# Kernel tuning notes

Hardware: AMD Instinct MI355X
Metric: run time of the kernel (lower is better)

## Reference

```python
import numpy as np
import jax
import jax.numpy as jnp
from collections import deque

NUM_CLASSES = 32
N_PARENTS = 4
N_CHILD = 7
SINK_WEIGHT = 0.1
EPS = 1e-7
B, D, H, W = 2, 96, 96, 96

# ---- static tree construction (mirrors adjacency_matrix / bitpack_tree / reachability) ----

def _build_adjacency():
    n = NUM_CLASSES + 1  # node 0 is the virtual root
    A = np.zeros((n, n), dtype=np.int64)
    for p in range(N_PARENTS):
        A[0, 1 + p] = 1
        for c in range(N_CHILD):
            A[1 + p, 1 + N_PARENTS + p * N_CHILD + c] = 1
    return A

ADJ = _build_adjacency()

def _reachability(A):
    # R[i, j] = 1 iff j is reachable from i (i is ancestor-or-self of j)
    R = np.eye(A.shape[0], dtype=bool) | (A > 0)
    for _ in range(A.shape[0]):
        Rn = R | (R @ (A > 0))
        if (Rn == R).all():
            break
        R = Rn
    return R

def _bitpack(A):
    # each node's bitmask encodes its path from the root; (x & group) == class tests descendant-ness
    n = A.shape[0]
    bc = np.zeros(n, dtype=np.int64)
    bg = np.zeros(n, dtype=np.int64)
    bit = 0
    q = deque([0])
    while q:
        p = q.popleft()
        ch = np.nonzero(A[p])[0]
        if len(ch) == 0:
            continue
        w = int(np.ceil(np.log2(len(ch) + 1)))
        for i, c in enumerate(ch):
            bc[c] = bc[p] | ((i + 1) << bit)
            bg[c] = bg[p] | (((1 << w) - 1) << bit)
            q.append(c)
        bit += w
    return bc, bg

_BC, _BG = _bitpack(ADJ)
BM_CLASS = _BC[1:].astype(np.int32)
BM_GROUP = _BG[1:].astype(np.int32)
RMT = _reachability(ADJ)[1:, 1:].T.astype(np.float32)  # RMT[label, c] = c is ancestor-or-self
LEAF = np.nonzero(ADJ[1:, 1:].sum(axis=1) == 0)[0].astype(np.int32)
_SIB = ((ADJ.T @ ADJ) > 0)[1:, 1:]
SINK_IDS = [N_PARENTS + p * N_CHILD for p in range(N_PARENTS)]
PARENT_OF = {s: int(ADJ[1:, 1:][:, s].argmax()) for s in SINK_IDS}
SIBS = {}
for _s in SINK_IDS:
    _row = _SIB[_s].copy()
    _row[_s] = False
    SIBS[_s] = np.nonzero(_row)[0].tolist()
# DDESC[l, c] = 1 iff class l is a descendant-or-self of class c (bitmask test)
DDESC = ((BM_CLASS[:, None] & BM_GROUP[None, :]) == BM_CLASS[None, :]).astype(np.float32)


def setup_inputs() -> dict:
    key = jax.random.key(0)
    k1, k2 = jax.random.split(key)
    images = jax.random.normal(k1, (B, NUM_CLASSES, D, H, W), dtype=jnp.float32)
    targets = jax.random.randint(k2, (B, D, H, W), 0, NUM_CLASSES, dtype=jnp.int32)
    masks = jnp.ones((B, NUM_CLASSES), dtype=bool)
    return {"images": images, "targets": targets, "masks": masks}


def reference(images, targets, masks):
    C = NUM_CLASSES
    probs = jax.nn.softmax(images, axis=1)  # activation_fn over class dim
    leaf = jnp.asarray(LEAF)
    pred = leaf[jnp.argmax(probs[:, LEAF], axis=1)]  # _argmax_leaves -> [B,D,H,W] int32
    bm_class = jnp.asarray(BM_CLASS)
    rmt = jnp.asarray(RMT)
    ddesc = jnp.asarray(DDESC)

    def per_sample(p, pr, y, m):
        p = p.reshape(C, -1).T          # [N, C] probabilities
        y = y.reshape(-1)
        pr = pr.reshape(-1)
        valid = y != 255
        vw = valid.astype(p.dtype)
        y_safe = jnp.where(valid, y, 0).astype(jnp.int32)
        mf = m.astype(p.dtype)

        # ---- sink dice (hierarchical sink/sibling logic) ----
        pred_bm = bm_class[pr]
        sds, fls = [], []
        for s in SINK_IDS:
            sib_mask = jnp.zeros_like(valid)
            for sib in SIBS[s]:
                sib_mask = sib_mask | (y_safe == sib) | ((~m[sib]) & (pr == sib))
            par = PARENT_OF[s]
            pmask = (pred_bm & int(BM_GROUP[par])) == int(BM_CLASS[par])
            tgt = (pmask & (~sib_mask)).astype(p.dtype) * vw
            pp = p[:, s] * vw
            inter = jnp.sum(pp * tgt)
            d = 1.0 - (2.0 * inter + 1e-5) / (jnp.sum(pp) + jnp.sum(tgt) + 1e-5)
            sds.append(d)
            fls.append((jnp.sum(sib_mask & valid) > 0).astype(p.dtype))
        sd = jnp.stack(sds)
        fl = jnp.stack(fls)
        cnt = fl.sum()
        sink_dice = SINK_WEIGHT * jnp.where(cnt > 0, jnp.sum(sd * fl) / jnp.maximum(cnt, 1.0), 0.0)

        # ---- main dice (smooth_nr=0) + hierarchical CE over masked classes ----
        t = rmt[y_safe]                 # [N, C] multi-hot (label + ancestors)
        wcol = vw[:, None]
        inter = jnp.sum(p * t * wcol, axis=0)
        denom = jnp.sum(p * wcol, axis=0) + jnp.sum(t * wcol, axis=0)
        dice_c = 1.0 - (2.0 * inter) / (denom + 1e-5)
        dice = jnp.sum(dice_c * mf) / jnp.maximum(mf.sum(), 1.0)

        logp = jnp.log(jnp.clip(p, EPS, 1.0 - EPS))
        ce = jnp.sum(-jnp.sum(t * logp * mf[None, :], axis=1) * vw) / jnp.maximum(vw.sum(), 1.0)

        # ---- confusion matrix via joint (pred, true) histogram + descendant matrix ----
        flat = pr.astype(jnp.int32) * C + y_safe
        hist = jnp.zeros((C * C,), p.dtype).at[flat].add(vw).reshape(C, C)  # [pred, true]
        tp = jnp.einsum('lc,lt,tc->c', ddesc, hist, ddesc)
        fp = jnp.einsum('lc,lt->c', ddesc, hist) - tp
        fn = jnp.einsum('lt,tc->c', hist, ddesc) - tp
        cm = jnp.stack([tp, fp, fn], axis=-1) * mf[:, None]
        return jnp.stack([ce, dice, sink_dice]), cm

    loss, cm = jax.vmap(per_sample)(probs, pred, targets, masks)
    return loss, cm, pred
```

## Files before the change

kernel.cpp:

```cpp
#include <hip/hip_runtime.h>

#define NC 32
#define NVOX (96*96*96)
#define NB 512
#define TPB 256
#define ROWS 33

#define WS_CE     0
#define WS_SP     32
#define WS_SPT    64
#define WS_SINKI  96
#define WS_SIB    100
#define WS_TGT    104
#define WS_HIST   128
#define SLOT_STRIDE 1152
#define NSLOT     (2 * NB)
#define FINAL_OFF (NSLOT * SLOT_STRIDE)
#define NCHUNK    8
#define BLK_PER_CH (NB / NCHUNK)

__device__ __forceinline__ float wave_reduce(float v) {
    #pragma unroll
    for (int off = 32; off > 0; off >>= 1)
        v += __shfl_down(v, off, 64);
    return v;
}

__global__ __launch_bounds__(TPB, 4) void voxel_kernel(
    const float* __restrict__ images,
    const int*   __restrict__ targets,
    const int*   __restrict__ masks,
    float* __restrict__ ws,
    float* __restrict__ pred_out)
{
    const int slot = blockIdx.x;
    const int b    = slot & 1;
    const int blk  = slot >> 1;
    const int tid  = threadIdx.x;

    __shared__ float s_e[TPB * ROWS];
    __shared__ float s_hist[NC * NC];
    __shared__ float s_spt[NC];
    __shared__ float s_mf[NC];
    __shared__ float s_red[45];

    for (int i = tid; i < NC * NC; i += TPB) s_hist[i] = 0.f;
    if (tid < 45) s_red[tid] = 0.f;
    if (tid < NC) {
        s_spt[tid] = 0.f;
        s_mf[tid]  = (masks[b * NC + tid] != 0) ? 1.f : 0.f;
    }
    __syncthreads();

    const float* img  = images + (size_t)b * NC * NVOX;
    const int*   tgt  = targets + (size_t)b * NVOX;
    float*       pout = pred_out + (size_t)b * NVOX;
    float*       wsb  = ws + (size_t)slot * SLOT_STRIDE;
    float*       et   = &s_e[tid * ROWS];

    float sp[NC];
    #pragma unroll
    for (int c = 0; c < NC; ++c) sp[c] = 0.f;
    float ce = 0.f;
    float sinkI[4] = {0.f, 0.f, 0.f, 0.f};
    float sibc[4]  = {0.f, 0.f, 0.f, 0.f};
    float tgtc[4]  = {0.f, 0.f, 0.f, 0.f};

    for (int v = blk * TPB + tid; v < NVOX; v += NB * TPB) {
        const int  y     = tgt[v];
        const bool valid = (y != 255);
        const int  ysafe = valid ? y : 0;
        const float vwf  = valid ? 1.f : 0.f;

        float sum  = 0.f;
        float best = -3.4e38f;
        int   pred = 4;
        #pragma unroll
        for (int c = 0; c < NC; ++c) {
            const float x  = img[(size_t)c * NVOX + v];
            const float ev = __expf(x);
            et[c] = ev;
            sum  += ev;
            if (c >= 4) {
                if (x > best) { best = x; pred = c; }
            }
        }
        const float rinv = 1.f / sum;
        pout[v] = (float)pred;

        const int pp = (pred - 4) / 7;
        const int py = (ysafe >= 4) ? (ysafe - 4) / 7 : -1;
        const int pyi = (py >= 0) ? py : 0;

        const float pyv  = et[ysafe] * rinv;
        const float ppv  = et[pyi] * rinv;
        const float eskv = et[4 + 7 * pp] * rinv;

        float term = __logf(fminf(fmaxf(pyv, 1e-7f), 1.f - 1e-7f)) * s_mf[ysafe];
        if (py >= 0)
            term += __logf(fminf(fmaxf(ppv, 1e-7f), 1.f - 1e-7f)) * s_mf[pyi];
        ce -= term * vwf;

        atomicAdd(&s_spt[ysafe], pyv * vwf);
        if (py >= 0) atomicAdd(&s_spt[pyi], ppv * vwf);

        atomicAdd(&s_hist[pred * NC + ysafe], vwf);

        const bool pm = (s_mf[pred] == 0.f);
        #pragma unroll
        for (int k = 0; k < 4; ++k) {
            const int  sk   = 4 + 7 * k;
            const bool ysib = (py == k) && (ysafe != sk);
            const bool msib = pm && (pp == k) && (pred != sk);
            const bool sib  = ysib || msib;
            if (sib && valid) sibc[k] += 1.f;
            if ((pp == k) && !sib && valid) {
                tgtc[k]  += 1.f;
                sinkI[k] += eskv;
            }
        }

        const float rw = rinv * vwf;
        #pragma unroll
        for (int c = 0; c < NC; ++c)
            sp[c] = __builtin_fmaf(et[c], rw, sp[c]);
    }

    const int lane = tid & 63;
    {
        float r = wave_reduce(ce);
        if (lane == 0) atomicAdd(&s_red[0], r);
    }
    #pragma unroll
    for (int c = 0; c < NC; ++c) {
        float r = wave_reduce(sp[c]);
        if (lane == 0) atomicAdd(&s_red[1 + c], r);
    }
    #pragma unroll
    for (int k = 0; k < 4; ++k) {
        float r = wave_reduce(sinkI[k]);
        if (lane == 0) atomicAdd(&s_red[33 + k], r);
        r = wave_reduce(sibc[k]);
        if (lane == 0) atomicAdd(&s_red[37 + k], r);
        r = wave_reduce(tgtc[k]);
        if (lane == 0) atomicAdd(&s_red[41 + k], r);
    }
    __syncthreads();

    for (int i = tid; i < NC * NC; i += TPB) wsb[WS_HIST + i] = s_hist[i];
    if (tid == 0) wsb[WS_CE] = s_red[0];
    if (tid < NC) {
        wsb[WS_SP  + tid] = s_red[1 + tid];
        wsb[WS_SPT + tid] = s_spt[tid];
    }
    if (tid < 4) {
        wsb[WS_SINKI + tid] = s_red[33 + tid];
        wsb[WS_SIB   + tid] = s_red[37 + tid];
        wsb[WS_TGT   + tid] = s_red[41 + tid];
    }
}

__global__ __launch_bounds__(TPB) void reduce_kernel(
    const float* __restrict__ ws, float* __restrict__ wsf)
{
    const int v = blockIdx.x * TPB + threadIdx.x;
    if (v >= 2 * SLOT_STRIDE) return;
    const int b   = v / SLOT_STRIDE;
    const int val = v % SLOT_STRIDE;
    const int blk0 = blockIdx.y * BLK_PER_CH;
    const float* base = ws + (size_t)b * SLOT_STRIDE + val;
    float s = 0.f;
    #pragma unroll 8
    for (int i = 0; i < BLK_PER_CH; ++i)
        s += base[(size_t)(2 * (blk0 + i)) * SLOT_STRIDE];
    atomicAdd(&wsf[v], s);
}

__global__ __launch_bounds__(64) void finalize_kernel(
    const float* __restrict__ wsf,
    const int*   __restrict__ masks,
    float* __restrict__ out)
{
    const int b = blockIdx.x;
    const float* wsb  = wsf + (size_t)b * SLOT_STRIDE;
    const float* hist = wsb + WS_HIST;
    const int tid = threadIdx.x;

    __shared__ float s_col[NC], s_row[NC], s_dice[NC], s_mf[NC];

    if (tid < NC) {
        float cs = 0.f, rs = 0.f;
        for (int j = 0; j < NC; ++j) {
            cs += hist[j * NC + tid];
            rs += hist[tid * NC + j];
        }
        s_col[tid] = cs;
        s_row[tid] = rs;
        s_mf[tid]  = (masks[b * NC + tid] != 0) ? 1.f : 0.f;
    }
    __syncthreads();

    if (tid < NC) {
        const int c = tid;
        float ycnt, pcnt, tp;
        if (c < 4) {
            int idx[8];
            idx[0] = c;
            for (int j = 0; j < 7; ++j) idx[1 + j] = 4 + 7 * c + j;
            ycnt = s_col[c]; pcnt = s_row[c];
            for (int j = 0; j < 7; ++j) { ycnt += s_col[idx[1 + j]]; pcnt += s_row[idx[1 + j]]; }
            tp = 0.f;
            for (int a = 0; a < 8; ++a)
                for (int d = 0; d < 8; ++d)
                    tp += hist[idx[a] * NC + idx[d]];
        } else {
            ycnt = s_col[c]; pcnt = s_row[c];
            tp = hist[c * NC + c];
        }
        const float mf = s_mf[c];
        out[6 + (b * NC + c) * 3 + 0] = tp * mf;
        out[6 + (b * NC + c) * 3 + 1] = (pcnt - tp) * mf;
        out[6 + (b * NC + c) * 3 + 2] = (ycnt - tp) * mf;
        float dc = 1.f - 2.f * wsb[WS_SPT + c] / (wsb[WS_SP + c] + ycnt + 1e-5f);
        s_dice[c] = dc * mf;
    }
    __syncthreads();

    if (tid == 0) {
        float vw = 0.f, dsum = 0.f, msum = 0.f;
        for (int c = 0; c < NC; ++c) {
            vw   += s_col[c];
            dsum += s_dice[c];
            msum += s_mf[c];
        }
        const float ce   = wsb[WS_CE] / fmaxf(vw, 1.f);
        const float dice = dsum / fmaxf(msum, 1.f);
        float cnt = 0.f, sd = 0.f;
        for (int k = 0; k < 4; ++k) {
            float fl = (wsb[WS_SIB + k] > 0.f) ? 1.f : 0.f;
            float d  = 1.f - (2.f * wsb[WS_SINKI + k] + 1e-5f) /
                             (wsb[WS_SP + 4 + 7 * k] + wsb[WS_TGT + k] + 1e-5f);
            cnt += fl;
            sd  += d * fl;
        }
        const float sink = (cnt > 0.f) ? 0.1f * (sd / fmaxf(cnt, 1.f)) : 0.f;
        out[b * 3 + 0] = ce;
        out[b * 3 + 1] = dice;
        out[b * 3 + 2] = sink;
    }
}

extern "C" void kernel_launch(void* const* d_in, const int* in_sizes, int n_in,
                              void* d_out, int out_size, void* d_ws, size_t ws_size,
                              hipStream_t stream) {
    const float* images  = (const float*)d_in[0];
    const int*   targets = (const int*)d_in[1];
    const int*   masks   = (const int*)d_in[2];
    float* out = (float*)d_out;
    float* ws  = (float*)d_ws;
    float* wsf = ws + FINAL_OFF;

    hipMemsetAsync(wsf, 0, 2 * SLOT_STRIDE * sizeof(float), stream);

    voxel_kernel<<<dim3(NSLOT), dim3(TPB), 0, stream>>>(
        images, targets, masks, ws, out + 6 + 2 * NC * 3);
    reduce_kernel<<<dim3((2 * SLOT_STRIDE + TPB - 1) / TPB, NCHUNK), dim3(TPB), 0, stream>>>(ws, wsf);
    finalize_kernel<<<dim3(2), dim3(64), 0, stream>>>(wsf, masks, out);
}
```

Measured before the change: 340.8 us.

## Keep softmax exponentials in registers and fuse finalize into reduce kernel

Drops the per-thread shared-memory exp buffer (33 floats per thread, about 33KB per block) and keeps the exponentials in a register array. The needed entries (target prob, parent prob, predicted sink prob) are picked up with selects inside the channel loop. This lifts the LDS limit on occupancy but raises register pressure. It also folds the finalize step into the reduce kernel using a last-block atomic counter, and moves the workspace zeroing into the voxel kernel, which removes a memset and a kernel launch.

```diff
diff --git a/kernel.cpp b/kernel.cpp
--- a/kernel.cpp
+++ b/kernel.cpp
@@ -4,7 +4,6 @@
 #define NVOX (96*96*96)
 #define NB 512
 #define TPB 256
-#define ROWS 33
 
 #define WS_CE     0
 #define WS_SP     32
@@ -16,8 +15,11 @@
 #define SLOT_STRIDE 1152
 #define NSLOT     (2 * NB)
 #define FINAL_OFF (NSLOT * SLOT_STRIDE)
+#define CTR_IDX   124
 #define NCHUNK    8
 #define BLK_PER_CH (NB / NCHUNK)
+#define RED_BLK_X ((2 * SLOT_STRIDE + TPB - 1) / TPB)
+#define RED_NBLK  (RED_BLK_X * NCHUNK)
 
 __device__ __forceinline__ float wave_reduce(float v) {
     #pragma unroll
@@ -38,7 +40,6 @@
     const int blk  = slot >> 1;
     const int tid  = threadIdx.x;
 
-    __shared__ float s_e[TPB * ROWS];
     __shared__ float s_hist[NC * NC];
     __shared__ float s_spt[NC];
     __shared__ float s_mf[NC];
@@ -50,13 +51,17 @@
         s_spt[tid] = 0.f;
         s_mf[tid]  = (masks[b * NC + tid] != 0) ? 1.f : 0.f;
     }
+    if (slot == 0) {
+        float* wsf = ws + FINAL_OFF;
+        for (int i = tid; i < 2 * SLOT_STRIDE; i += TPB) wsf[i] = 0.f;
+        if (tid == 0) *(unsigned int*)(ws + CTR_IDX) = 0u;
+    }
     __syncthreads();
 
     const float* img  = images + (size_t)b * NC * NVOX;
     const int*   tgt  = targets + (size_t)b * NVOX;
     float*       pout = pred_out + (size_t)b * NVOX;
     float*       wsb  = ws + (size_t)slot * SLOT_STRIDE;
-    float*       et   = &s_e[tid * ROWS];
 
     float sp[NC];
     #pragma unroll
@@ -71,30 +76,38 @@
         const bool valid = (y != 255);
         const int  ysafe = valid ? y : 0;
         const float vwf  = valid ? 1.f : 0.f;
-
-        float sum  = 0.f;
-        float best = -3.4e38f;
+        const int  py    = (ysafe >= 4) ? (ysafe - 4) / 7 : -1;
+        const int  pyi   = (py >= 0) ? py : 0;
+
+        float ev[NC];
+        float sum = 0.f, best = -3.4e38f;
+        float pyv_e = 0.f, ppv_e = 0.f, cur = 0.f, esk = 0.f;
         int   pred = 4;
         #pragma unroll
         for (int c = 0; c < NC; ++c) {
-            const float x  = img[(size_t)c * NVOX + v];
-            const float ev = __expf(x);
-            et[c] = ev;
-            sum  += ev;
+            const float x = img[(size_t)c * NVOX + v];
+            const float e = __expf(x);
+            ev[c] = e;
+            sum  += e;
+            pyv_e = (c == ysafe) ? e : pyv_e;
+            if (c < 4)
+                ppv_e = (c == pyi) ? e : ppv_e;
+            if (c >= 4 && ((c - 4) % 7) == 0)
+                cur = e;
             if (c >= 4) {
-                if (x > best) { best = x; pred = c; }
+                const bool g = (x > best);
+                best = g ? x : best;
+                pred = g ? c : pred;
+                esk  = g ? cur : esk;
             }
         }
         const float rinv = 1.f / sum;
         pout[v] = (float)pred;
 
         const int pp = (pred - 4) / 7;
-        const int py = (ysafe >= 4) ? (ysafe - 4) / 7 : -1;
-        const int pyi = (py >= 0) ? py : 0;
-
-        const float pyv  = et[ysafe] * rinv;
-        const float ppv  = et[pyi] * rinv;
-        const float eskv = et[4 + 7 * pp] * rinv;
+        const float pyv  = pyv_e * rinv;
+        const float ppv  = ppv_e * rinv;
+        const float eskv = esk   * rinv;
 
         float term = __logf(fminf(fmaxf(pyv, 1e-7f), 1.f - 1e-7f)) * s_mf[ysafe];
         if (py >= 0)
@@ -123,7 +136,7 @@
         const float rw = rinv * vwf;
         #pragma unroll
         for (int c = 0; c < NC; ++c)
-            sp[c] = __builtin_fmaf(et[c], rw, sp[c]);
+            sp[c] = __builtin_fmaf(ev[c], rw, sp[c]);
     }
 
     const int lane = tid & 63;
@@ -161,79 +174,87 @@
 }
 
 __global__ __launch_bounds__(TPB) void reduce_kernel(
-    const float* __restrict__ ws, float* __restrict__ wsf)
+    const float* __restrict__ ws,
+    float* __restrict__ wsf,
+    const int* __restrict__ masks,
+    float* __restrict__ out,
+    unsigned int* __restrict__ ctr)
 {
     const int v = blockIdx.x * TPB + threadIdx.x;
-    if (v >= 2 * SLOT_STRIDE) return;
-    const int b   = v / SLOT_STRIDE;
-    const int val = v % SLOT_STRIDE;
-    const int blk0 = blockIdx.y * BLK_PER_CH;
-    const float* base = ws + (size_t)b * SLOT_STRIDE + val;
-    float s = 0.f;
-    #pragma unroll 8
-    for (int i = 0; i < BLK_PER_CH; ++i)
-        s += base[(size_t)(2 * (blk0 + i)) * SLOT_STRIDE];
-    atomicAdd(&wsf[v], s);
-}
-
-__global__ __launch_bounds__(64) void finalize_kernel(
-    const float* __restrict__ wsf,
-    const int*   __restrict__ masks,
-    float* __restrict__ out)
-{
-    const int b = blockIdx.x;
-    const float* wsb  = wsf + (size_t)b * SLOT_STRIDE;
-    const float* hist = wsb + WS_HIST;
-    const int tid = threadIdx.x;
-
-    __shared__ float s_col[NC], s_row[NC], s_dice[NC], s_mf[NC];
-
-    if (tid < NC) {
+    {
+        const int b    = v / SLOT_STRIDE;
+        const int val  = v % SLOT_STRIDE;
+        const int blk0 = blockIdx.y * BLK_PER_CH;
+        const float* base = ws + (size_t)b * SLOT_STRIDE + val;
+        float s = 0.f;
+        #pragma unroll 8
+        for (int i = 0; i < BLK_PER_CH; ++i)
+            s += base[(size_t)(2 * (blk0 + i)) * SLOT_STRIDE];
+        atomicAdd(&wsf[v], s);
+    }
+
+    __shared__ unsigned int s_last;
+    __threadfence();
+    __syncthreads();
+    if (threadIdx.x == 0) s_last = atomicAdd(ctr, 1u);
+    __syncthreads();
+    if (s_last != RED_NBLK - 1) return;
+    __threadfence();
+
+    __shared__ float f_col[2][NC], f_row[2][NC], f_dice[2][NC], f_mf[2][NC];
+    const int t  = threadIdx.x & 63;
+    const int fb = threadIdx.x >> 6;
+    const bool act = (fb < 2) && (t < NC);
+
+    if (act) {
+        const float* hist = wsf + (size_t)fb * SLOT_STRIDE + WS_HIST;
         float cs = 0.f, rs = 0.f;
         for (int j = 0; j < NC; ++j) {
-            cs += hist[j * NC + tid];
-            rs += hist[tid * NC + j];
-        }
-        s_col[tid] = cs;
-        s_row[tid] = rs;
-        s_mf[tid]  = (masks[b * NC + tid] != 0) ? 1.f : 0.f;
-    }
-    __syncthreads();
-
-    if (tid < NC) {
-        const int c = tid;
+            cs += hist[j * NC + t];
+            rs += hist[t * NC + j];
+        }
+        f_col[fb][t] = cs;
+        f_row[fb][t] = rs;
+        f_mf[fb][t]  = (masks[fb * NC + t] != 0) ? 1.f : 0.f;
+    }
+    __syncthreads();
+
+    if (act) {
+        const float* wsb  = wsf + (size_t)fb * SLOT_STRIDE;
+        const float* hist = wsb + WS_HIST;
+        const int c = t;
         float ycnt, pcnt, tp;
         if (c < 4) {
             int idx[8];
             idx[0] = c;
             for (int j = 0; j < 7; ++j) idx[1 + j] = 4 + 7 * c + j;
-            ycnt = s_col[c]; pcnt = s_row[c];
-            for (int j = 0; j < 7; ++j) { ycnt += s_col[idx[1 + j]]; pcnt += s_row[idx[1 + j]]; }
+            ycnt = f_col[fb][c]; pcnt = f_row[fb][c];
+            for (int j = 0; j < 7; ++j) { ycnt += f_col[fb][idx[1 + j]]; pcnt += f_row[fb][idx[1 + j]]; }
             tp = 0.f;
             for (int a = 0; a < 8; ++a)
                 for (int d = 0; d < 8; ++d)
                     tp += hist[idx[a] * NC + idx[d]];
         } else {
-            ycnt = s_col[c]; pcnt = s_row[c];
+            ycnt = f_col[fb][c]; pcnt = f_row[fb][c];
             tp = hist[c * NC + c];
         }
-        const float mf = s_mf[c];
-        out[6 + (b * NC + c) * 3 + 0] = tp * mf;
-        out[6 + (b * NC + c) * 3 + 1] = (pcnt - tp) * mf;
-        out[6 + (b * NC + c) * 3 + 2] = (ycnt - tp) * mf;
-        float dc = 1.f - 2.f * wsb[WS_SPT + c] / (wsb[WS_SP + c] + ycnt + 1e-5f);
-        s_dice[c] = dc * mf;
-    }
-    __syncthreads();
-
-    if (tid == 0) {
+        const float mf = f_mf[fb][c];
+        out[6 + (fb * NC + c) * 3 + 0] = tp * mf;
+        out[6 + (fb * NC + c) * 3 + 1] = (pcnt - tp) * mf;
+        out[6 + (fb * NC + c) * 3 + 2] = (ycnt - tp) * mf;
+        f_dice[fb][c] = (1.f - 2.f * wsb[WS_SPT + c] / (wsb[WS_SP + c] + ycnt + 1e-5f)) * mf;
+    }
+    __syncthreads();
+
+    if (fb < 2 && t == 0) {
+        const float* wsb = wsf + (size_t)fb * SLOT_STRIDE;
         float vw = 0.f, dsum = 0.f, msum = 0.f;
         for (int c = 0; c < NC; ++c) {
-            vw   += s_col[c];
-            dsum += s_dice[c];
-            msum += s_mf[c];
-        }
-        const float ce   = wsb[WS_CE] / fmaxf(vw, 1.f);
+            vw   += f_col[fb][c];
+            dsum += f_dice[fb][c];
+            msum += f_mf[fb][c];
+        }
+        const float cel  = wsb[WS_CE] / fmaxf(vw, 1.f);
         const float dice = dsum / fmaxf(msum, 1.f);
         float cnt = 0.f, sd = 0.f;
         for (int k = 0; k < 4; ++k) {
@@ -243,10 +264,9 @@
             cnt += fl;
             sd  += d * fl;
         }
-        const float sink = (cnt > 0.f) ? 0.1f * (sd / fmaxf(cnt, 1.f)) : 0.f;
-        out[b * 3 + 0] = ce;
-        out[b * 3 + 1] = dice;
-        out[b * 3 + 2] = sink;
+        out[fb * 3 + 0] = cel;
+        out[fb * 3 + 1] = dice;
+        out[fb * 3 + 2] = (cnt > 0.f) ? 0.1f * (sd / fmaxf(cnt, 1.f)) : 0.f;
     }
 }
 
@@ -260,10 +280,8 @@
     float* ws  = (float*)d_ws;
     float* wsf = ws + FINAL_OFF;
 
-    hipMemsetAsync(wsf, 0, 2 * SLOT_STRIDE * sizeof(float), stream);
-
     voxel_kernel<<<dim3(NSLOT), dim3(TPB), 0, stream>>>(
         images, targets, masks, ws, out + 6 + 2 * NC * 3);
-    reduce_kernel<<<dim3((2 * SLOT_STRIDE + TPB - 1) / TPB, NCHUNK), dim3(TPB), 0, stream>>>(ws, wsf);
-    finalize_kernel<<<dim3(2), dim3(64), 0, stream>>>(wsf, masks, out);
-}
+    reduce_kernel<<<dim3(RED_BLK_X, NCHUNK), dim3(TPB), 0, stream>>>(
+        ws, wsf, masks, out, (unsigned int*)(ws + CTR_IDX));
+}
```

Measured after the change: 344.0 us. No clear change (+0.9%).
